# Kernel optimization log

Hardware: AMD Instinct MI355X
Metric: run time of the kernel (lower is better)

The kernel has to match this reference:

```python
import jax, jax.numpy as jnp
import numpy as np

D = 256
N_EDGES = 8192
N_CORNERS = 4096


def setup_inputs() -> dict:
    key = jax.random.key(0)
    ks = jax.random.split(key, 8)
    scale = 1.0 / np.sqrt(D)
    return {
        "edge_pred": jax.random.uniform(ks[0], (N_EDGES,), dtype=jnp.float32),
        "edge_corner": jax.random.randint(ks[1], (N_EDGES, 2), 0, N_CORNERS, dtype=jnp.int64),
        "all_corners": jax.random.uniform(ks[2], (N_CORNERS, 2), dtype=jnp.float32),
        "edge_x": jax.random.normal(ks[3], (N_EDGES, D), dtype=jnp.float32),
        "image_x": jax.random.normal(ks[4], (1024,), dtype=jnp.float32),
        "W1": jax.random.normal(ks[5], (D, D), dtype=jnp.float32) * scale,
        "b1": jnp.zeros((D,), dtype=jnp.float32),
        "W2": jax.random.normal(ks[6], (D, D), dtype=jnp.float32) * scale,
        "b2": jnp.zeros((D,), dtype=jnp.float32),
        "W3": jax.random.normal(ks[7], (3 * D, D), dtype=jnp.float32) * scale,
        "b3": jnp.zeros((D,), dtype=jnp.float32),
    }


def _linear_block(x, W, b):
    # LinearBlock: Linear followed by ReLU
    return jax.nn.relu(x @ W + b)


def reference(edge_pred, edge_corner, all_corners, edge_x, image_x, W1, b1, W2, b2, W3, b3):
    # 'fully' branch of MPModule.forward. edge_pred/edge_corner/all_corners/image_x
    # are unused in this branch (kept for signature fidelity).
    e1 = _linear_block(edge_x, W1, b1)              # [N, D]
    # (e1.unsqueeze(1) * e1).mean(-1) == (e1 @ e1.T) / D   -> [N, N]
    sim1 = (e1 @ e1.T) / D
    e2 = _linear_block(edge_x, W2, b2)
    sim2 = (e2 @ e2.T) / D
    # (edge_x * sim.unsqueeze(-1)).sum(1) == sim @ edge_x  -> [N, D]
    agg1 = sim1 @ edge_x
    agg2 = sim2 @ edge_x
    cat = jnp.concatenate([edge_x, agg1, agg2], axis=-1)  # [N, 3D]
    out = _linear_block(cat, W3, b3)                      # [N, D]
    return out
```

## Files before the change

### kernel.cpp

```cpp
#include <hip/hip_runtime.h>

#define NE 8192
#define DD 256
#define NSPLIT 32

typedef __attribute__((ext_vector_type(8))) short short8;
typedef __attribute__((ext_vector_type(4))) short short4v;
typedef __attribute__((ext_vector_type(8))) __bf16 bf16x8;
typedef __attribute__((ext_vector_type(4))) float floatx4;

__device__ __forceinline__ unsigned short f2bf(float f) {
  union { float f; unsigned int i; } v; v.f = f;
  unsigned int r = v.i + 0x7fffu + ((v.i >> 16) & 1u);
  return (unsigned short)(r >> 16);
}

__device__ __forceinline__ floatx4 mfma_bf16(short8 a, short8 b, floatx4 c) {
  return __builtin_amdgcn_mfma_f32_16x16x32_bf16(
      __builtin_bit_cast(bf16x8, a), __builtin_bit_cast(bf16x8, b), c, 0, 0, 0);
}

__device__ __forceinline__ void tcvt_tile(const float* __restrict__ src, int C,
                                          unsigned short* __restrict__ dst, int R,
                                          int r0, int c0, int tid) {
  __shared__ float ls[64][68];
  const int rr = tid >> 4;
  const int c4 = (tid & 15) * 4;
#pragma unroll
  for (int k = 0; k < 4; ++k)
    *(floatx4*)&ls[rr + k * 16][c4] =
        *(const floatx4*)&src[(size_t)(r0 + rr + k * 16) * C + c0 + c4];
  __syncthreads();
  const int cc = tid >> 2;
  const int rb = (tid & 3) * 16;
  short8 o0, o1;
#pragma unroll
  for (int i = 0; i < 8; ++i) {
    o0[i] = (short)f2bf(ls[rb + i][cc]);
    o1[i] = (short)f2bf(ls[rb + 8 + i][cc]);
  }
  unsigned short* dp = &dst[(size_t)(c0 + cc) * R + r0 + rb];
  *(short8*)dp = o0;
  *(short8*)(dp + 8) = o1;
}

__global__ void cvt_all(const float* __restrict__ x, unsigned short* __restrict__ xb,
                        unsigned short* __restrict__ xT,
                        const float* __restrict__ W1, unsigned short* __restrict__ W1t,
                        const float* __restrict__ W2, unsigned short* __restrict__ W2t,
                        const float* __restrict__ W3, unsigned short* __restrict__ W3t0) {
  const int b = blockIdx.x, tid = threadIdx.x;
  if (b < 1024) {
    int i = b * 256 + tid;
    floatx4 a = ((const floatx4*)x)[2 * i];
    floatx4 c = ((const floatx4*)x)[2 * i + 1];
    short8 o;
#pragma unroll
    for (int k = 0; k < 4; ++k) { o[k] = (short)f2bf(a[k]); o[4 + k] = (short)f2bf(c[k]); }
    ((short8*)xb)[i] = o;
  } else if (b < 1536) {
    int t = b - 1024;
    tcvt_tile(x, DD, xT, NE, (t >> 2) * 64, (t & 3) * 64, tid);
  } else if (b < 1552) {
    int t = b - 1536;
    tcvt_tile(W1, DD, W1t, DD, (t >> 2) * 64, (t & 3) * 64, tid);
  } else if (b < 1568) {
    int t = b - 1552;
    tcvt_tile(W2, DD, W2t, DD, (t >> 2) * 64, (t & 3) * 64, tid);
  } else {
    int t = b - 1568;
    tcvt_tile(W3, DD, W3t0, DD, (t >> 2) * 64, (t & 3) * 64, tid);
  }
}

__global__ __launch_bounds__(256, 3)
void e_gemm(const unsigned short* __restrict__ xb,
            const unsigned short* __restrict__ W1t, const float* __restrict__ b1,
            const unsigned short* __restrict__ W2t, const float* __restrict__ b2,
            unsigned short* __restrict__ e1, unsigned short* __restrict__ e2,
            unsigned short* __restrict__ e1T, unsigned short* __restrict__ e2T)
{
  __shared__ __align__(16) unsigned short smA[64 * 136];
  __shared__ __align__(16) unsigned short smB1[64 * 136];
  __shared__ __align__(16) unsigned short smB2[64 * 136];
  const int T = threadIdx.x, lane = T & 63, wv = T >> 6;
  const int q = lane >> 4, r = lane & 15;
  const int col0 = blockIdx.x * 64, row0 = blockIdx.y * 64;

  floatx4 acc1[4], acc2[4];
#pragma unroll
  for (int j = 0; j < 4; ++j) {
    acc1[j] = (floatx4){0.f, 0.f, 0.f, 0.f};
    acc2[j] = (floatx4){0.f, 0.f, 0.f, 0.f};
  }

  for (int kc = 0; kc < 256; kc += 128) {
#pragma unroll
    for (int p = 0; p < 4; ++p) {
      const int id = p * 256 + T, rr = id >> 4, k8 = (id & 15) * 8;
      *(short8*)&smA[rr * 136 + k8] =
          *(const short8*)&xb[(size_t)(row0 + rr) * DD + kc + k8];
      *(short8*)&smB1[rr * 136 + k8] =
          *(const short8*)&W1t[(size_t)(col0 + rr) * DD + kc + k8];
      *(short8*)&smB2[rr * 136 + k8] =
          *(const short8*)&W2t[(size_t)(col0 + rr) * DD + kc + k8];
    }
    __syncthreads();
#pragma unroll
    for (int ks = 0; ks < 4; ++ks) {
      short8 af = *(const short8*)&smA[(wv * 16 + r) * 136 + ks * 32 + q * 8];
#pragma unroll
      for (int j = 0; j < 4; ++j) {
        short8 b1f = *(const short8*)&smB1[(j * 16 + r) * 136 + ks * 32 + q * 8];
        short8 b2f = *(const short8*)&smB2[(j * 16 + r) * 136 + ks * 32 + q * 8];
        acc1[j] = mfma_bf16(af, b1f, acc1[j]);
        acc2[j] = mfma_bf16(af, b2f, acc2[j]);
      }
    }
    __syncthreads();
  }

#pragma unroll
  for (int j = 0; j < 4; ++j) {
    const int col = col0 + j * 16 + r;
    const int rowb = row0 + wv * 16 + q * 4;
    const float b1v = b1[col], b2v = b2[col];
    short4v t1, t2;
#pragma unroll
    for (int t = 0; t < 4; ++t) {
      unsigned short h1 = f2bf(fmaxf(acc1[j][t] + b1v, 0.0f));
      unsigned short h2 = f2bf(fmaxf(acc2[j][t] + b2v, 0.0f));
      t1[t] = (short)h1; t2[t] = (short)h2;
      e1[(size_t)(rowb + t) * DD + col] = h1;
      e2[(size_t)(rowb + t) * DD + col] = h2;
    }
    *(short4v*)&e1T[(size_t)col * NE + rowb] = t1;
    *(short4v*)&e2T[(size_t)col * NE + rowb] = t2;
  }
}

__global__ __launch_bounds__(256, 3)
void atb(const unsigned short* __restrict__ e1T, const unsigned short* __restrict__ e2T,
         const unsigned short* __restrict__ xT, float* __restrict__ P_T)
{
  __shared__ __align__(16) unsigned short smA[128 * 136];
  __shared__ __align__(16) unsigned short smB[64 * 136];
  const int T = threadIdx.x, lane = T & 63, wv = T >> 6;
  const int q = lane >> 4, r = lane & 15;
  const int m0 = (blockIdx.x >> 2) * 128, n0 = (blockIdx.x & 3) * 64;
  const int y = blockIdx.y, z = blockIdx.z;
  const int j0 = y * (NE / NSPLIT);
  const unsigned short* E = z ? e2T : e1T;
  float* P = P_T + (size_t)(z * NSPLIT + y) * 65536;

  floatx4 acc[2][4];
#pragma unroll
  for (int i = 0; i < 2; ++i)
#pragma unroll
    for (int j = 0; j < 4; ++j) acc[i][j] = (floatx4){0.f, 0.f, 0.f, 0.f};

  for (int jc = 0; jc < NE / NSPLIT; jc += 128) {
#pragma unroll
    for (int p = 0; p < 8; ++p) {
      const int id = p * 256 + T, mm = id >> 4, j8 = (id & 15) * 8;
      *(short8*)&smA[mm * 136 + j8] =
          *(const short8*)&E[(size_t)(m0 + mm) * NE + j0 + jc + j8];
    }
#pragma unroll
    for (int p = 0; p < 4; ++p) {
      const int id = p * 256 + T, nn = id >> 4, j8 = (id & 15) * 8;
      *(short8*)&smB[nn * 136 + j8] =
          *(const short8*)&xT[(size_t)(n0 + nn) * NE + j0 + jc + j8];
    }
    __syncthreads();
#pragma unroll
    for (int ks = 0; ks < 4; ++ks) {
      short8 af[2], bf[4];
#pragma unroll
      for (int i = 0; i < 2; ++i)
        af[i] = *(const short8*)&smA[(wv * 32 + i * 16 + r) * 136 + ks * 32 + q * 8];
#pragma unroll
      for (int j = 0; j < 4; ++j)
        bf[j] = *(const short8*)&smB[(j * 16 + r) * 136 + ks * 32 + q * 8];
#pragma unroll
      for (int i = 0; i < 2; ++i)
#pragma unroll
        for (int j = 0; j < 4; ++j)
          acc[i][j] = mfma_bf16(af[i], bf[j], acc[i][j]);
    }
    __syncthreads();
  }
#pragma unroll
  for (int i = 0; i < 2; ++i)
#pragma unroll
    for (int j = 0; j < 4; ++j) {
      const int n = n0 + j * 16 + r;
      const int m = m0 + wv * 32 + i * 16 + q * 4;
      *(floatx4*)&P[(size_t)n * DD + m] = acc[i][j];
    }
}

__global__ void reduce_g(const float* __restrict__ P_T, float* __restrict__ G_T) {
  int idx = blockIdx.x * 256 + threadIdx.x;
  int z = idx >> 14, off = idx & 16383;
  const floatx4* Pp = (const floatx4*)P_T;
  floatx4 s = (floatx4){0.f, 0.f, 0.f, 0.f};
#pragma unroll
  for (int y = 0; y < NSPLIT; ++y)
    s += Pp[(size_t)(z * NSPLIT + y) * 16384 + off];
  ((floatx4*)G_T)[idx] = s;
}

__global__ __launch_bounds__(256, 2)
void h_mfma(const float* __restrict__ G_T, const float* __restrict__ W3,
            unsigned short* __restrict__ H1t, unsigned short* __restrict__ H2t)
{
  __shared__ __align__(16) unsigned short smA[64 * 136];
  __shared__ __align__(16) unsigned short smB[64 * 136];
  const int T = threadIdx.x, lane = T & 63, wv = T >> 6;
  const int q = lane >> 4, r = lane & 15;
  const int z = blockIdx.z;
  const int me0 = (blockIdx.x >> 2) * 64, m30 = (blockIdx.x & 3) * 64;
  const float* G = G_T + (size_t)z * 65536;
  unsigned short* Ht = z ? H2t : H1t;
  const int woff = 256 + z * 256;

  floatx4 acc[4];
#pragma unroll
  for (int j = 0; j < 4; ++j) acc[j] = (floatx4){0.f, 0.f, 0.f, 0.f};

  for (int lc = 0; lc < 256; lc += 128) {
#pragma unroll
    for (int p = 0; p < 2; ++p) {
      const int id = p * 256 + T, lb = id >> 4, e4 = id & 15;
      floatx4 grow[4], wrow[4];
#pragma unroll
      for (int i = 0; i < 4; ++i) {
        grow[i] = *(const floatx4*)&G[(size_t)(lc + lb * 4 + i) * DD + me0 + e4 * 4];
        wrow[i] = *(const floatx4*)&W3[(size_t)(woff + lc + lb * 4 + i) * DD + m30 + e4 * 4];
      }
#pragma unroll
      for (int s4 = 0; s4 < 4; ++s4) {
        const int c = (s4 + e4) & 3;
        short4v ga = {(short)f2bf(grow[0][c] * 0.00390625f),
                      (short)f2bf(grow[1][c] * 0.00390625f),
                      (short)f2bf(grow[2][c] * 0.00390625f),
                      (short)f2bf(grow[3][c] * 0.00390625f)};
        short4v wa = {(short)f2bf(wrow[0][c]), (short)f2bf(wrow[1][c]),
                      (short)f2bf(wrow[2][c]), (short)f2bf(wrow[3][c])};
        *(short4v*)&smA[(e4 * 4 + c) * 136 + lb * 4] = ga;
        *(short4v*)&smB[(e4 * 4 + c) * 136 + lb * 4] = wa;
      }
    }
    __syncthreads();
#pragma unroll
    for (int ks = 0; ks < 4; ++ks) {
      short8 af = *(const short8*)&smA[(wv * 16 + r) * 136 + ks * 32 + q * 8];
#pragma unroll
      for (int j = 0; j < 4; ++j) {
        short8 bf = *(const short8*)&smB[(j * 16 + r) * 136 + ks * 32 + q * 8];
        acc[j] = mfma_bf16(af, bf, acc[j]);
      }
    }
    __syncthreads();
  }
#pragma unroll
  for (int j = 0; j < 4; ++j) {
    const int m3 = m30 + j * 16 + r;
    const int me = me0 + wv * 16 + q * 4;
    short4v v;
#pragma unroll
    for (int i = 0; i < 4; ++i) v[i] = (short)f2bf(acc[j][i]);
    *(short4v*)&Ht[(size_t)m3 * DD + me] = v;
  }
}

__global__ __launch_bounds__(256, 3)
void out_gemm(const unsigned short* __restrict__ xb,
              const unsigned short* __restrict__ e1, const unsigned short* __restrict__ e2,
              const unsigned short* __restrict__ W3t0,
              const unsigned short* __restrict__ H1t, const unsigned short* __restrict__ H2t,
              const float* __restrict__ b3, float* __restrict__ out)
{
  __shared__ __align__(16) unsigned short smA[64 * 136];
  __shared__ __align__(16) unsigned short smB[64 * 136];
  const int T = threadIdx.x, lane = T & 63, wv = T >> 6;
  const int q = lane >> 4, r = lane & 15;
  const int col0 = blockIdx.x * 64, row0 = blockIdx.y * 64;

  floatx4 acc[4];
#pragma unroll
  for (int j = 0; j < 4; ++j) acc[j] = (floatx4){0.f, 0.f, 0.f, 0.f};

  const unsigned short* As[3] = {xb, e1, e2};
  const unsigned short* Bs[3] = {W3t0, H1t, H2t};

  for (int rd = 0; rd < 6; ++rd) {
    const int s = rd >> 1, kc = (rd & 1) * 128;
    const unsigned short* A = As[s];
    const unsigned short* B = Bs[s];
#pragma unroll
    for (int p = 0; p < 4; ++p) {
      const int id = p * 256 + T, rr = id >> 4, k8 = (id & 15) * 8;
      *(short8*)&smA[rr * 136 + k8] =
          *(const short8*)&A[(size_t)(row0 + rr) * DD + kc + k8];
      *(short8*)&smB[rr * 136 + k8] =
          *(const short8*)&B[(size_t)(col0 + rr) * DD + kc + k8];
    }
    __syncthreads();
#pragma unroll
    for (int ks = 0; ks < 4; ++ks) {
      short8 af = *(const short8*)&smA[(wv * 16 + r) * 136 + ks * 32 + q * 8];
#pragma unroll
      for (int j = 0; j < 4; ++j) {
        short8 bf = *(const short8*)&smB[(j * 16 + r) * 136 + ks * 32 + q * 8];
        acc[j] = mfma_bf16(af, bf, acc[j]);
      }
    }
    __syncthreads();
  }
#pragma unroll
  for (int j = 0; j < 4; ++j) {
    const int col = col0 + j * 16 + r;
    const float bv = b3[col];
    const int rowb = row0 + wv * 16 + q * 4;
#pragma unroll
    for (int t = 0; t < 4; ++t)
      out[(size_t)(rowb + t) * DD + col] = fmaxf(acc[j][t] + bv, 0.0f);
  }
}

extern "C" void kernel_launch(void* const* d_in, const int* in_sizes, int n_in,
                              void* d_out, int out_size, void* d_ws, size_t ws_size,
                              hipStream_t stream) {
  (void)in_sizes; (void)n_in; (void)out_size; (void)ws_size;
  const float* x  = (const float*)d_in[3];
  const float* W1 = (const float*)d_in[5];
  const float* b1 = (const float*)d_in[6];
  const float* W2 = (const float*)d_in[7];
  const float* b2 = (const float*)d_in[8];
  const float* W3 = (const float*)d_in[9];
  const float* b3 = (const float*)d_in[10];
  float* out = (float*)d_out;

  char* ws = (char*)d_ws;
  const size_t MB = 1u << 20;
  const size_t KB = 1u << 10;
  unsigned short* xb   = (unsigned short*)ws;
  unsigned short* xT   = (unsigned short*)(ws + 4 * MB);
  unsigned short* e1   = (unsigned short*)(ws + 8 * MB);
  unsigned short* e2   = (unsigned short*)(ws + 12 * MB);
  unsigned short* e1T  = (unsigned short*)(ws + 16 * MB);
  unsigned short* e2T  = (unsigned short*)(ws + 20 * MB);
  unsigned short* W1t  = (unsigned short*)(ws + 24 * MB);
  unsigned short* W2t  = (unsigned short*)(ws + 24 * MB + 128 * KB);
  unsigned short* W3t0 = (unsigned short*)(ws + 24 * MB + 256 * KB);
  unsigned short* H1t  = (unsigned short*)(ws + 24 * MB + 384 * KB);
  unsigned short* H2t  = (unsigned short*)(ws + 24 * MB + 512 * KB);
  float* G_T           = (float*)(ws + 24 * MB + 640 * KB);
  float* P_T           = (float*)(ws + 25 * MB);

  cvt_all<<<1584, 256, 0, stream>>>(x, xb, xT, W1, W1t, W2, W2t, W3, W3t0);
  e_gemm<<<dim3(4, 128), 256, 0, stream>>>(xb, W1t, b1, W2t, b2, e1, e2, e1T, e2T);
  atb<<<dim3(8, NSPLIT, 2), 256, 0, stream>>>(e1T, e2T, xT, P_T);
  reduce_g<<<128, 256, 0, stream>>>(P_T, G_T);
  h_mfma<<<dim3(16, 1, 2), 256, 0, stream>>>(G_T, W3, H1t, H2t);
  out_gemm<<<dim3(4, 128), 256, 0, stream>>>(xb, e1, e2, W3t0, H1t, H2t, b3, out);
}
```

Baseline: 126.0 us.

## Register-prefetch GEMM tiles, fuse x conversion passes, retile atb split-K

Adds register-staged prefetching of the next K chunk in e_gemm, atb and out_gemm, so global loads for the next tile overlap the MFMA work on the current one. Merges the x-to-bf16 row conversion into the transpose tiles, so x is read once instead of twice. Shrinks the atb tile to 64x64, halves the split-K count and raises the occupancy hint to 4. The prefetch registers add pressure and may limit occupancy.

```diff
diff --git a/kernel.cpp b/kernel.cpp
--- a/kernel.cpp
+++ b/kernel.cpp
@@ -2,7 +2,7 @@
 
 #define NE 8192
 #define DD 256
-#define NSPLIT 32
+#define NSPLIT 16
 
 typedef __attribute__((ext_vector_type(8))) short short8;
 typedef __attribute__((ext_vector_type(4))) short short4v;
@@ -20,24 +20,22 @@
       __builtin_bit_cast(bf16x8, a), __builtin_bit_cast(bf16x8, b), c, 0, 0, 0);
 }
 
-__device__ __forceinline__ void tcvt_tile(const float* __restrict__ src, int C,
+__device__ __forceinline__ void tcvt_tile(float* ls,
+                                          const float* __restrict__ src, int C,
                                           unsigned short* __restrict__ dst, int R,
                                           int r0, int c0, int tid) {
-  __shared__ float ls[64][68];
-  const int rr = tid >> 4;
-  const int c4 = (tid & 15) * 4;
+  const int rr = tid >> 4, c4 = (tid & 15) * 4;
 #pragma unroll
   for (int k = 0; k < 4; ++k)
-    *(floatx4*)&ls[rr + k * 16][c4] =
+    *(floatx4*)&ls[(rr + k * 16) * 68 + c4] =
         *(const floatx4*)&src[(size_t)(r0 + rr + k * 16) * C + c0 + c4];
   __syncthreads();
-  const int cc = tid >> 2;
-  const int rb = (tid & 3) * 16;
+  const int cc = tid >> 2, rb = (tid & 3) * 16;
   short8 o0, o1;
 #pragma unroll
   for (int i = 0; i < 8; ++i) {
-    o0[i] = (short)f2bf(ls[rb + i][cc]);
-    o1[i] = (short)f2bf(ls[rb + 8 + i][cc]);
+    o0[i] = (short)f2bf(ls[(rb + i) * 68 + cc]);
+    o1[i] = (short)f2bf(ls[(rb + 8 + i) * 68 + cc]);
   }
   unsigned short* dp = &dst[(size_t)(c0 + cc) * R + r0 + rb];
   *(short8*)dp = o0;
@@ -49,27 +47,37 @@
                         const float* __restrict__ W1, unsigned short* __restrict__ W1t,
                         const float* __restrict__ W2, unsigned short* __restrict__ W2t,
                         const float* __restrict__ W3, unsigned short* __restrict__ W3t0) {
+  __shared__ float ls[64 * 68];
   const int b = blockIdx.x, tid = threadIdx.x;
-  if (b < 1024) {
-    int i = b * 256 + tid;
-    floatx4 a = ((const floatx4*)x)[2 * i];
-    floatx4 c = ((const floatx4*)x)[2 * i + 1];
-    short8 o;
-#pragma unroll
-    for (int k = 0; k < 4; ++k) { o[k] = (short)f2bf(a[k]); o[4 + k] = (short)f2bf(c[k]); }
-    ((short8*)xb)[i] = o;
-  } else if (b < 1536) {
-    int t = b - 1024;
-    tcvt_tile(x, DD, xT, NE, (t >> 2) * 64, (t & 3) * 64, tid);
-  } else if (b < 1552) {
-    int t = b - 1536;
-    tcvt_tile(W1, DD, W1t, DD, (t >> 2) * 64, (t & 3) * 64, tid);
-  } else if (b < 1568) {
-    int t = b - 1552;
-    tcvt_tile(W2, DD, W2t, DD, (t >> 2) * 64, (t & 3) * 64, tid);
+  if (b < 512) {
+    const int r0 = (b >> 2) * 64, c0 = (b & 3) * 64;
+    const int rr = tid >> 4, c4 = (tid & 15) * 4;
+#pragma unroll
+    for (int k = 0; k < 4; ++k) {
+      floatx4 v = *(const floatx4*)&x[(size_t)(r0 + rr + k * 16) * DD + c0 + c4];
+      *(floatx4*)&ls[(rr + k * 16) * 68 + c4] = v;
+      short4v s;
+#pragma unroll
+      for (int c = 0; c < 4; ++c) s[c] = (short)f2bf(v[c]);
+      *(short4v*)&xb[(size_t)(r0 + rr + k * 16) * DD + c0 + c4] = s;
+    }
+    __syncthreads();
+    const int cc = tid >> 2, rb = (tid & 3) * 16;
+    short8 o0, o1;
+#pragma unroll
+    for (int i = 0; i < 8; ++i) {
+      o0[i] = (short)f2bf(ls[(rb + i) * 68 + cc]);
+      o1[i] = (short)f2bf(ls[(rb + 8 + i) * 68 + cc]);
+    }
+    unsigned short* dp = &xT[(size_t)(c0 + cc) * NE + r0 + rb];
+    *(short8*)dp = o0;
+    *(short8*)(dp + 8) = o1;
   } else {
-    int t = b - 1568;
-    tcvt_tile(W3, DD, W3t0, DD, (t >> 2) * 64, (t & 3) * 64, tid);
+    int t = b - 512;
+    const float* src = (t < 16) ? W1 : ((t < 32) ? W2 : W3);
+    unsigned short* dst = (t < 16) ? W1t : ((t < 32) ? W2t : W3t0);
+    t &= 15;
+    tcvt_tile(ls, src, DD, dst, DD, (t >> 2) * 64, (t & 3) * 64, tid);
   }
 }
 
@@ -94,18 +102,33 @@
     acc2[j] = (floatx4){0.f, 0.f, 0.f, 0.f};
   }
 
+  short8 pa[4], pb1[4], pb2[4];
+#pragma unroll
+  for (int p = 0; p < 4; ++p) {
+    const int id = p * 256 + T, rr = id >> 4, k8 = (id & 15) * 8;
+    pa[p]  = *(const short8*)&xb[(size_t)(row0 + rr) * DD + k8];
+    pb1[p] = *(const short8*)&W1t[(size_t)(col0 + rr) * DD + k8];
+    pb2[p] = *(const short8*)&W2t[(size_t)(col0 + rr) * DD + k8];
+  }
+
   for (int kc = 0; kc < 256; kc += 128) {
 #pragma unroll
     for (int p = 0; p < 4; ++p) {
       const int id = p * 256 + T, rr = id >> 4, k8 = (id & 15) * 8;
-      *(short8*)&smA[rr * 136 + k8] =
-          *(const short8*)&xb[(size_t)(row0 + rr) * DD + kc + k8];
-      *(short8*)&smB1[rr * 136 + k8] =
-          *(const short8*)&W1t[(size_t)(col0 + rr) * DD + kc + k8];
-      *(short8*)&smB2[rr * 136 + k8] =
-          *(const short8*)&W2t[(size_t)(col0 + rr) * DD + kc + k8];
-    }
-    __syncthreads();
+      *(short8*)&smA[rr * 136 + k8]  = pa[p];
+      *(short8*)&smB1[rr * 136 + k8] = pb1[p];
+      *(short8*)&smB2[rr * 136 + k8] = pb2[p];
+    }
+    __syncthreads();
+    if (kc + 128 < 256) {
+#pragma unroll
+      for (int p = 0; p < 4; ++p) {
+        const int id = p * 256 + T, rr = id >> 4, k8 = (id & 15) * 8;
+        pa[p]  = *(const short8*)&xb[(size_t)(row0 + rr) * DD + kc + 128 + k8];
+        pb1[p] = *(const short8*)&W1t[(size_t)(col0 + rr) * DD + kc + 128 + k8];
+        pb2[p] = *(const short8*)&W2t[(size_t)(col0 + rr) * DD + kc + 128 + k8];
+      }
+    }
 #pragma unroll
     for (int ks = 0; ks < 4; ++ks) {
       short8 af = *(const short8*)&smA[(wv * 16 + r) * 136 + ks * 32 + q * 8];
@@ -139,65 +162,65 @@
   }
 }
 
-__global__ __launch_bounds__(256, 3)
+__global__ __launch_bounds__(256, 4)
 void atb(const unsigned short* __restrict__ e1T, const unsigned short* __restrict__ e2T,
          const unsigned short* __restrict__ xT, float* __restrict__ P_T)
 {
-  __shared__ __align__(16) unsigned short smA[128 * 136];
+  __shared__ __align__(16) unsigned short smA[64 * 136];
   __shared__ __align__(16) unsigned short smB[64 * 136];
   const int T = threadIdx.x, lane = T & 63, wv = T >> 6;
   const int q = lane >> 4, r = lane & 15;
-  const int m0 = (blockIdx.x >> 2) * 128, n0 = (blockIdx.x & 3) * 64;
+  const int m0 = (blockIdx.x >> 2) * 64, n0 = (blockIdx.x & 3) * 64;
   const int y = blockIdx.y, z = blockIdx.z;
   const int j0 = y * (NE / NSPLIT);
   const unsigned short* E = z ? e2T : e1T;
   float* P = P_T + (size_t)(z * NSPLIT + y) * 65536;
 
-  floatx4 acc[2][4];
-#pragma unroll
-  for (int i = 0; i < 2; ++i)
-#pragma unroll
-    for (int j = 0; j < 4; ++j) acc[i][j] = (floatx4){0.f, 0.f, 0.f, 0.f};
+  floatx4 acc[4];
+#pragma unroll
+  for (int j = 0; j < 4; ++j) acc[j] = (floatx4){0.f, 0.f, 0.f, 0.f};
+
+  short8 pa[4], pb[4];
+#pragma unroll
+  for (int p = 0; p < 4; ++p) {
+    const int id = p * 256 + T, mm = id >> 4, j8 = (id & 15) * 8;
+    pa[p] = *(const short8*)&E[(size_t)(m0 + mm) * NE + j0 + j8];
+    pb[p] = *(const short8*)&xT[(size_t)(n0 + mm) * NE + j0 + j8];
+  }
 
   for (int jc = 0; jc < NE / NSPLIT; jc += 128) {
 #pragma unroll
-    for (int p = 0; p < 8; ++p) {
+    for (int p = 0; p < 4; ++p) {
       const int id = p * 256 + T, mm = id >> 4, j8 = (id & 15) * 8;
-      *(short8*)&smA[mm * 136 + j8] =
-          *(const short8*)&E[(size_t)(m0 + mm) * NE + j0 + jc + j8];
-    }
-#pragma unroll
-    for (int p = 0; p < 4; ++p) {
-      const int id = p * 256 + T, nn = id >> 4, j8 = (id & 15) * 8;
-      *(short8*)&smB[nn * 136 + j8] =
-          *(const short8*)&xT[(size_t)(n0 + nn) * NE + j0 + jc + j8];
-    }
-    __syncthreads();
+      *(short8*)&smA[mm * 136 + j8] = pa[p];
+      *(short8*)&smB[mm * 136 + j8] = pb[p];
+    }
+    __syncthreads();
+    if (jc + 128 < NE / NSPLIT) {
+#pragma unroll
+      for (int p = 0; p < 4; ++p) {
+        const int id = p * 256 + T, mm = id >> 4, j8 = (id & 15) * 8;
+        pa[p] = *(const short8*)&E[(size_t)(m0 + mm) * NE + j0 + jc + 128 + j8];
+        pb[p] = *(const short8*)&xT[(size_t)(n0 + mm) * NE + j0 + jc + 128 + j8];
+      }
+    }
 #pragma unroll
     for (int ks = 0; ks < 4; ++ks) {
-      short8 af[2], bf[4];
-#pragma unroll
-      for (int i = 0; i < 2; ++i)
-        af[i] = *(const short8*)&smA[(wv * 32 + i * 16 + r) * 136 + ks * 32 + q * 8];
-#pragma unroll
-      for (int j = 0; j < 4; ++j)
-        bf[j] = *(const short8*)&smB[(j * 16 + r) * 136 + ks * 32 + q * 8];
-#pragma unroll
-      for (int i = 0; i < 2; ++i)
-#pragma unroll
-        for (int j = 0; j < 4; ++j)
-          acc[i][j] = mfma_bf16(af[i], bf[j], acc[i][j]);
-    }
-    __syncthreads();
-  }
-#pragma unroll
-  for (int i = 0; i < 2; ++i)
-#pragma unroll
-    for (int j = 0; j < 4; ++j) {
-      const int n = n0 + j * 16 + r;
-      const int m = m0 + wv * 32 + i * 16 + q * 4;
-      *(floatx4*)&P[(size_t)n * DD + m] = acc[i][j];
-    }
+      short8 af = *(const short8*)&smA[(wv * 16 + r) * 136 + ks * 32 + q * 8];
+#pragma unroll
+      for (int j = 0; j < 4; ++j) {
+        short8 bf = *(const short8*)&smB[(j * 16 + r) * 136 + ks * 32 + q * 8];
+        acc[j] = mfma_bf16(af, bf, acc[j]);
+      }
+    }
+    __syncthreads();
+  }
+#pragma unroll
+  for (int j = 0; j < 4; ++j) {
+    const int n = n0 + j * 16 + r;
+    const int m = m0 + wv * 16 + q * 4;
+    *(floatx4*)&P[(size_t)n * DD + m] = acc[j];
+  }
 }
 
 __global__ void reduce_g(const float* __restrict__ P_T, float* __restrict__ G_T) {
@@ -275,7 +298,7 @@
   }
 }
 
-__global__ __launch_bounds__(256, 3)
+__global__ __launch_bounds__(256, 4)
 void out_gemm(const unsigned short* __restrict__ xb,
               const unsigned short* __restrict__ e1, const unsigned short* __restrict__ e2,
               const unsigned short* __restrict__ W3t0,
@@ -288,26 +311,40 @@
   const int q = lane >> 4, r = lane & 15;
   const int col0 = blockIdx.x * 64, row0 = blockIdx.y * 64;
 
-  floatx4 acc[4];
-#pragma unroll
-  for (int j = 0; j < 4; ++j) acc[j] = (floatx4){0.f, 0.f, 0.f, 0.f};
-
   const unsigned short* As[3] = {xb, e1, e2};
   const unsigned short* Bs[3] = {W3t0, H1t, H2t};
 
+  floatx4 acc[4];
+#pragma unroll
+  for (int j = 0; j < 4; ++j) acc[j] = (floatx4){0.f, 0.f, 0.f, 0.f};
+
+  short8 qa[4], qb[4];
+#pragma unroll
+  for (int p = 0; p < 4; ++p) {
+    const int id = p * 256 + T, rr = id >> 4, k8 = (id & 15) * 8;
+    qa[p] = *(const short8*)&As[0][(size_t)(row0 + rr) * DD + k8];
+    qb[p] = *(const short8*)&Bs[0][(size_t)(col0 + rr) * DD + k8];
+  }
+
   for (int rd = 0; rd < 6; ++rd) {
-    const int s = rd >> 1, kc = (rd & 1) * 128;
-    const unsigned short* A = As[s];
-    const unsigned short* B = Bs[s];
 #pragma unroll
     for (int p = 0; p < 4; ++p) {
       const int id = p * 256 + T, rr = id >> 4, k8 = (id & 15) * 8;
-      *(short8*)&smA[rr * 136 + k8] =
-          *(const short8*)&A[(size_t)(row0 + rr) * DD + kc + k8];
-      *(short8*)&smB[rr * 136 + k8] =
-          *(const short8*)&B[(size_t)(col0 + rr) * DD + kc + k8];
-    }
-    __syncthreads();
+      *(short8*)&smA[rr * 136 + k8] = qa[p];
+      *(short8*)&smB[rr * 136 + k8] = qb[p];
+    }
+    __syncthreads();
+    if (rd + 1 < 6) {
+      const int s = (rd + 1) >> 1, kc = ((rd + 1) & 1) * 128;
+      const unsigned short* A = As[s];
+      const unsigned short* B = Bs[s];
+#pragma unroll
+      for (int p = 0; p < 4; ++p) {
+        const int id = p * 256 + T, rr = id >> 4, k8 = (id & 15) * 8;
+        qa[p] = *(const short8*)&A[(size_t)(row0 + rr) * DD + kc + k8];
+        qb[p] = *(const short8*)&B[(size_t)(col0 + rr) * DD + kc + k8];
+      }
+    }
 #pragma unroll
     for (int ks = 0; ks < 4; ++ks) {
       short8 af = *(const short8*)&smA[(wv * 16 + r) * 136 + ks * 32 + q * 8];
@@ -360,9 +397,9 @@
   float* G_T           = (float*)(ws + 24 * MB + 640 * KB);
   float* P_T           = (float*)(ws + 25 * MB);
 
-  cvt_all<<<1584, 256, 0, stream>>>(x, xb, xT, W1, W1t, W2, W2t, W3, W3t0);
+  cvt_all<<<560, 256, 0, stream>>>(x, xb, xT, W1, W1t, W2, W2t, W3, W3t0);
   e_gemm<<<dim3(4, 128), 256, 0, stream>>>(xb, W1t, b1, W2t, b2, e1, e2, e1T, e2T);
-  atb<<<dim3(8, NSPLIT, 2), 256, 0, stream>>>(e1T, e2T, xT, P_T);
+  atb<<<dim3(16, NSPLIT, 2), 256, 0, stream>>>(e1T, e2T, xT, P_T);
   reduce_g<<<128, 256, 0, stream>>>(P_T, G_T);
   h_mfma<<<dim3(16, 1, 2), 256, 0, stream>>>(G_T, W3, H1t, H2t);
   out_gemm<<<dim3(4, 128), 256, 0, stream>>>(xb, e1, e2, W3t0, H1t, H2t, b3, out);
```

After: 122.1 us. 3.1% less time.
